# Kernel optimization log

Measured on AMD Instinct MI355X. Metric: run time of the kernel, lower is better.

The kernel has to match this reference:

```python
import jax, jax.numpy as jnp
import numpy as np

EPS = 1e-5  # torch LayerNorm default
H = 8       # heads_num


def _ln(t, g, b):
    m = jnp.mean(t, axis=-1, keepdims=True)
    v = jnp.var(t, axis=-1, keepdims=True)
    return (t - m) / jnp.sqrt(v + EPS) * g + b


def setup_inputs() -> dict:
    key = jax.random.key(0)
    ks = jax.random.split(key, 12)
    B, S, Dq, Dk, Dff = 4, 2048, 512, 768, 2048
    def w(k, shape, scale=0.02):
        return jax.random.normal(k, shape, jnp.float32) * scale
    return {
        "x": jax.random.normal(ks[0], (B, S, Dq), jnp.float32),
        "y": jax.random.normal(ks[1], (B, S, Dk), jnp.float32),
        # cross-attention projections (stored [in, out]; linear_q/k/v have no bias)
        "Wq": w(ks[2], (Dq, Dq)), "Wk": w(ks[3], (Dk, Dq)), "Wv": w(ks[4], (Dk, Dq)),
        "Wo": w(ks[5], (Dq, Dq)), "bo": jnp.zeros((Dq,), jnp.float32),
        # nn.MultiheadAttention packed in-projection and out-projection
        "mha_w_in": w(ks[6], (Dq, 3 * Dq)), "mha_b_in": jnp.zeros((3 * Dq,), jnp.float32),
        "mha_wo": w(ks[7], (Dq, Dq)), "mha_bo": jnp.zeros((Dq,), jnp.float32),
        # 4 LayerNorms
        "ln1_g": jnp.ones((Dq,), jnp.float32), "ln1_b": jnp.zeros((Dq,), jnp.float32),
        "ln2_g": jnp.ones((Dk,), jnp.float32), "ln2_b": jnp.zeros((Dk,), jnp.float32),
        "ln3_g": jnp.ones((Dq,), jnp.float32), "ln3_b": jnp.zeros((Dq,), jnp.float32),
        "ln4_g": jnp.ones((Dq,), jnp.float32), "ln4_b": jnp.zeros((Dq,), jnp.float32),
        # dense MLP (moe=False branch)
        "mlp_w1": w(ks[8], (Dq, Dff)), "mlp_b1": jnp.zeros((Dff,), jnp.float32),
        "mlp_w2": w(ks[9], (Dff, Dq)), "mlp_b2": jnp.zeros((Dq,), jnp.float32),
    }


def reference(x, y, Wq, Wk, Wv, Wo, bo, mha_w_in, mha_b_in, mha_wo, mha_bo,
              ln1_g, ln1_b, ln2_g, ln2_b, ln3_g, ln3_b, ln4_g, ln4_b,
              mlp_w1, mlp_b1, mlp_w2, mlp_b2):
    B, S, D = x.shape
    hd = D // H
    inv_sqrt_hd = 1.0 / np.sqrt(hd).astype(np.float32)

    xn = _ln(x, ln1_g, ln1_b)
    yn = _ln(y, ln2_g, ln2_b)

    # ---- Multi_CrossAttention: manual QK^T softmax V over true seq axis ----
    q = (xn @ Wq).reshape(B, S, H, hd)
    k = (yn @ Wk).reshape(B, -1, H, hd)
    v = (yn @ Wv).reshape(B, -1, H, hd)
    scores = jnp.einsum('bqhd,bkhd->bhqk', q, k) * inv_sqrt_hd  # [B,H,S,S] (512 MB)
    attn = jax.nn.softmax(scores, axis=-1)
    ctx = jnp.einsum('bhqk,bkhd->bqhd', attn, v).reshape(B, S, D)
    ca = ctx @ Wo + bo

    h = _ln(ca + xn, ln3_g, ln3_b)

    # ---- nn.MultiheadAttention (batch_first=False!): axis 0 is the sequence ----
    qkv = h @ mha_w_in + mha_b_in  # [L=B, N=S, 3D]
    q2, k2, v2 = jnp.split(qkv, 3, axis=-1)
    L, N = q2.shape[0], q2.shape[1]
    q2 = q2.reshape(L, N, H, hd)
    k2 = k2.reshape(L, N, H, hd)
    v2 = v2.reshape(L, N, H, hd)
    s2 = jnp.einsum('lnhd,mnhd->nhlm', q2, k2) * inv_sqrt_hd  # [N,H,L,L]
    a2 = jax.nn.softmax(s2, axis=-1)
    sa = jnp.einsum('nhlm,mnhd->lnhd', a2, v2).reshape(L, N, D) @ mha_wo + mha_bo

    h2 = _ln(sa + h, ln4_g, ln4_b)

    # ---- dense MLP (GELU exact, dropout=0) ----
    mlp = jax.nn.gelu(h2 @ mlp_w1 + mlp_b1, approximate=False) @ mlp_w2 + mlp_b2
    return mlp + h2
```

## Files before the change

### kernel.cpp

```cpp
#include <hip/hip_runtime.h>
#include <math.h>

typedef unsigned short u16;
typedef __attribute__((ext_vector_type(8))) short bf8;
typedef __attribute__((ext_vector_type(4))) float f4;
typedef __attribute__((ext_vector_type(16))) float f32x16;
typedef __attribute__((ext_vector_type(4))) unsigned int u32x4;
typedef __attribute__((ext_vector_type(2))) unsigned int u32x2;
typedef __attribute__((ext_vector_type(4))) unsigned short u16x4;
typedef __attribute__((ext_vector_type(8))) unsigned short u16x8;

__device__ __forceinline__ float bf2f(u16 a){
  unsigned u = ((unsigned)a) << 16;
  float f; __builtin_memcpy(&f, &u, 4);
  return f;
}
__device__ __forceinline__ u16 f2bf(float f){
  unsigned u; __builtin_memcpy(&u, &f, 4);
  u += 0x7fffu + ((u >> 16) & 1u);
  return (u16)(u >> 16);
}
__device__ __forceinline__ unsigned cvtpk(float a, float b){
  unsigned r;
  asm("v_cvt_pk_bf16_f32 %0, %1, %2" : "=v"(r) : "v"(a), "v"(b));
  return r;
}
__device__ __forceinline__ void plswap(unsigned &a, unsigned &b){
  asm("v_permlane32_swap_b32 %0, %1" : "+v"(a), "+v"(b));
}
__device__ __forceinline__ void gload16(const u16* g, u16* l){
  __builtin_amdgcn_global_load_lds((const __attribute__((address_space(1))) void*)g,
                                   (__attribute__((address_space(3))) void*)l, 16, 0, 0);
}
__device__ __forceinline__ int xcd_swizzle(int orig, int nwg){
  const int qq = nwg >> 3, rr = nwg & 7;
  const int xcd = orig & 7, loc = orig >> 3;
  return (xcd < rr ? xcd * (qq + 1) : rr * (qq + 1) + (xcd - rr) * qq) + loc;
}

__global__ void k_transpose_all(
    const float* __restrict__ Wq, const float* __restrict__ Wk,
    const float* __restrict__ Wv, const float* __restrict__ Wo,
    const float* __restrict__ Win, const float* __restrict__ Wmo,
    const float* __restrict__ W1, const float* __restrict__ W2,
    u16* __restrict__ WqT, u16* __restrict__ WkT, u16* __restrict__ WvT,
    u16* __restrict__ WoT, u16* __restrict__ WinT, u16* __restrict__ WmoT,
    u16* __restrict__ W1T, u16* __restrict__ W2T)
{
  __shared__ float tile[32][33];
  const int tid = blockIdx.x;
  const float* in; u16* out; int R, C, lo;
  if (tid < 1280){
    if (tid < 256)       { in = Wq;  out = WqT;  R = 512; C = 512;  lo = 0; }
    else if (tid < 640)  { in = Wk;  out = WkT;  R = 768; C = 512;  lo = 256; }
    else if (tid < 1024) { in = Wv;  out = WvT;  R = 768; C = 512;  lo = 640; }
    else                 { in = Wo;  out = WoT;  R = 512; C = 512;  lo = 1024; }
  } else {
    if (tid < 2048)      { in = Win; out = WinT; R = 512; C = 1536; lo = 1280; }
    else if (tid < 2304) { in = Wmo; out = WmoT; R = 512; C = 512;  lo = 2048; }
    else if (tid < 3328) { in = W1;  out = W1T;  R = 512; C = 2048; lo = 2304; }
    else                 { in = W2;  out = W2T;  R = 2048; C = 512; lo = 3328; }
  }
  const int local = tid - lo;
  const int tpx = C >> 5;
  const int bx = (local % tpx) * 32, by = (local / tpx) * 32;
  const int tx = threadIdx.x, ty = threadIdx.y;
#pragma unroll
  for (int i = 0; i < 4; i++)
    tile[ty + i*8][tx] = in[(size_t)(by + ty + i*8) * C + bx + tx];
  __syncthreads();
#pragma unroll
  for (int i = 0; i < 4; i++)
    out[(size_t)(bx + ty + i*8) * R + by + tx] = f2bf(tile[tx][ty + i*8]);
}

__device__ __forceinline__ void ln_row(
    const float* __restrict__ r, const float* __restrict__ gam,
    const float* __restrict__ bet, float* __restrict__ outf,
    u16* __restrict__ outb, int D, int t)
{
  const int nv = D >> 8;
  float v[3] = {0.f, 0.f, 0.f};
  float s = 0.f, s2 = 0.f;
#pragma unroll
  for (int i = 0; i < 3; i++){
    if (i < nv){ float xx = r[t + i*256]; v[i] = xx; s += xx; s2 += xx*xx; }
  }
#pragma unroll
  for (int m = 32; m; m >>= 1){ s += __shfl_xor(s, m); s2 += __shfl_xor(s2, m); }
  __shared__ float rs[4], rq[4];
  const int wave = t >> 6;
  if ((t & 63) == 0){ rs[wave] = s; rq[wave] = s2; }
  __syncthreads();
  s  = rs[0] + rs[1] + rs[2] + rs[3];
  s2 = rq[0] + rq[1] + rq[2] + rq[3];
  const float mean = s / (float)D;
  const float var  = s2 / (float)D - mean * mean;
  const float rstd = rsqrtf(var + 1e-5f);
#pragma unroll
  for (int i = 0; i < 3; i++){
    if (i < nv){
      const int c = t + i*256;
      float o = (v[i] - mean) * rstd * gam[c] + bet[c];
      if (outf) outf[c] = o;
      outb[c] = f2bf(o);
    }
  }
}

__global__ __launch_bounds__(256) void k_layernorm(
    const float* __restrict__ in, const float* __restrict__ gam,
    const float* __restrict__ bet, float* __restrict__ outf,
    u16* __restrict__ outb, int D)
{
  const int row = blockIdx.x;
  ln_row(in + (size_t)row * D, gam, bet,
         outf ? outf + (size_t)row * D : nullptr,
         outb + (size_t)row * D, D, threadIdx.x);
}

__global__ __launch_bounds__(256) void k_layernorm12(
    const float* __restrict__ x, const float* __restrict__ y,
    const float* __restrict__ g1, const float* __restrict__ b1,
    const float* __restrict__ g2, const float* __restrict__ b2,
    float* __restrict__ xnF, u16* __restrict__ xnB, u16* __restrict__ ynB)
{
  const int row = blockIdx.x;
  if (row < 8192){
    ln_row(x + (size_t)row * 512, g1, b1, xnF + (size_t)row * 512,
           xnB + (size_t)row * 512, 512, threadIdx.x);
  } else {
    const int r2 = row - 8192;
    ln_row(y + (size_t)r2 * 768, g2, b2, nullptr,
           ynB + (size_t)r2 * 768, 768, threadIdx.x);
  }
}

template<int TM, int TN, bool BIAS, bool RES, bool GELU_ACT, int OUTM, bool QSC = false>
__global__ __launch_bounds__(256, 4) void k_gemm(
    const u16* __restrict__ A, const u16* __restrict__ BT,
    const float* __restrict__ bias, const float* __restrict__ res,
    float* __restrict__ outf, u16* __restrict__ outb, u16* __restrict__ outb2,
    int M, int N, int K)
{
  constexpr int MF = TM / 32;
  constexpr int NF = TN / 32;
  constexpr int WM = TM / 2;
  constexpr int WN = TN / 2;
  __shared__ u16 Sb[(TM + TN) * 64];
  const int t = threadIdx.x;
  const int gx = gridDim.x;
  const int swz = xcd_swizzle(blockIdx.y * gx + blockIdx.x, gx * gridDim.y);
  const int m0 = (swz / gx) * TM, n0 = (swz % gx) * TN;
  const int wave = t >> 6, lane = t & 63;
  const int wm = wave >> 1, wn = wave & 1;
  const int l15 = lane & 15, lg = lane >> 4;
  const u16* Ag = A + (size_t)m0 * K;
  const u16* Bg = BT + (size_t)n0 * K;

  const int lrow = lane >> 3;
  const int csrc = (((lane & 7) ^ lrow) << 3);
  const u16* Agl = Ag + (size_t)lrow * K + csrc;
  const u16* Bgl = Bg + (size_t)lrow * K + csrc;

  f4 acc[MF][NF];
#pragma unroll
  for (int i = 0; i < MF; i++)
#pragma unroll
    for (int j = 0; j < NF; j++) acc[i][j] = (f4){0.f, 0.f, 0.f, 0.f};

  const int nK = K >> 6;
#pragma unroll
  for (int i = 0; i < TM/32; i++){
    const int rb = (i*4 + wave) * 8;
    gload16(Agl + (size_t)rb * K, &Sb[rb * 64]);
  }
#pragma unroll
  for (int i = 0; i < TN/32; i++){
    const int rb = (i*4 + wave) * 8;
    gload16(Bgl + (size_t)rb * K, &Sb[(TM + rb) * 64]);
  }
  asm volatile("s_waitcnt vmcnt(0)" ::: "memory");
  __syncthreads();

  for (int kt = 0;; kt++){
    const char* As = (const char*)&Sb[0];
    const char* Bs = (const char*)&Sb[TM * 64];
#pragma unroll
    for (int kc = 0; kc < 2; kc++){
      bf8 af[MF], bfr[NF];
      const int kb = kc*64 + lg*16;
#pragma unroll
      for (int mf = 0; mf < MF; mf++){
        const int row = wm*WM + mf*16 + l15;
        af[mf] = *(const bf8*)(As + row*128 + (kb ^ ((row & 7) << 4)));
      }
#pragma unroll
      for (int nf = 0; nf < NF; nf++){
        const int row = wn*WN + nf*16 + l15;
        bfr[nf] = *(const bf8*)(Bs + row*128 + (kb ^ ((row & 7) << 4)));
      }
#pragma unroll
      for (int mf = 0; mf < MF; mf++)
#pragma unroll
        for (int nf = 0; nf < NF; nf++)
          acc[mf][nf] = __builtin_amdgcn_mfma_f32_16x16x32_bf16(af[mf], bfr[nf], acc[mf][nf], 0, 0, 0);
    }
    if (kt + 1 == nK) break;
    __syncthreads();
    const int ko = (kt + 1) << 6;
#pragma unroll
    for (int i = 0; i < TM/32; i++){
      const int rb = (i*4 + wave) * 8;
      gload16(Agl + (size_t)rb * K + ko, &Sb[rb * 64]);
    }
#pragma unroll
    for (int i = 0; i < TN/32; i++){
      const int rb = (i*4 + wave) * 8;
      gload16(Bgl + (size_t)rb * K + ko, &Sb[(TM + rb) * 64]);
    }
    asm volatile("s_waitcnt vmcnt(0)" ::: "memory");
    __syncthreads();
  }
#pragma unroll
  for (int mf = 0; mf < MF; mf++){
#pragma unroll
    for (int nf = 0; nf < NF; nf++){
      const int colg = n0 + wn*WN + nf*16 + l15;
      const int rowg = m0 + wm*WM + mf*16 + lg*4;
      const float bv = BIAS ? bias[colg] : 0.f;
      float vv[4];
#pragma unroll
      for (int j = 0; j < 4; j++){
        float v = acc[mf][nf][j] + bv;
        if (RES) v += res[(size_t)(rowg + j) * N + colg];
        if (GELU_ACT) v = 0.5f * v * (1.f + erff(v * 0.7071067811865475f));
        if (QSC) v *= 0.1803368801f;
        vv[j] = v;
      }
      if (OUTM == 0){
#pragma unroll
        for (int j = 0; j < 4; j++) outf[(size_t)(rowg + j) * N + colg] = vv[j];
      } else if (OUTM == 1){
#pragma unroll
        for (int j = 0; j < 4; j++) outb[(size_t)(rowg + j) * N + colg] = f2bf(vv[j]);
      } else if (OUTM == 2){
        const int bb = rowg >> 11, ss = rowg & 2047;
        u16x4 pk;
#pragma unroll
        for (int j = 0; j < 4; j++) pk[j] = f2bf(vv[j]);
        *(u16x4*)(outb + ((size_t)(bb*512 + colg)) * 2048 + ss) = pk;
      } else {
        if (n0 < 512){
#pragma unroll
          for (int j = 0; j < 4; j++) outb[(size_t)(rowg + j) * 512 + colg] = f2bf(vv[j]);
        } else {
          const int bb = rowg >> 11, ss = rowg & 2047;
          u16x4 pk;
#pragma unroll
          for (int j = 0; j < 4; j++) pk[j] = f2bf(vv[j]);
          *(u16x4*)(outb2 + ((size_t)(bb*512 + (colg - 512))) * 2048 + ss) = pk;
        }
      }
    }
  }
}

__global__ __launch_bounds__(256, 2) void k_flash(
    const u16* __restrict__ q, const u16* __restrict__ k,
    const u16* __restrict__ vt, u16* __restrict__ ctx)
{
  __shared__ u16 Kb[2][64 * 64];
  __shared__ u16 Vb[2][64 * 64];
  const int t = threadIdx.x;
  const int wave = t >> 6, lane = t & 63;
  const int l31 = lane & 31, hi = lane >> 5;
  const int id = blockIdx.y * 16 + blockIdx.x;
  const int swz = xcd_swizzle(id, 512);
  const int qb = swz & 15, bh = swz >> 4;
  const int b = bh >> 3, h = bh & 7;
  const int qrow0 = qb*128 + wave*32;

  bf8 qf[4];
  {
    const u16* qp = q + ((size_t)(b*2048 + qrow0 + l31)) * 512 + h*64 + hi*8;
    qf[0] = *(const bf8*)qp;
    qf[1] = *(const bf8*)(qp + 16);
    qf[2] = *(const bf8*)(qp + 32);
    qf[3] = *(const bf8*)(qp + 48);
  }

  const int lrow = lane >> 3;
  const int csrc = (((lane & 7) ^ lrow) << 3);
  const u16* kgl = k  + ((size_t)(b*2048 + lrow)) * 512  + h*64 + csrc;
  const u16* vgl = vt + ((size_t)(b*512 + h*64 + lrow)) * 2048 + csrc;

#pragma unroll
  for (int i = 0; i < 2; i++){
    const int rb = (i*4 + wave) * 8;
    gload16(kgl + (size_t)rb * 512,  &Kb[0][rb * 64]);
    gload16(vgl + (size_t)rb * 2048, &Vb[0][rb * 64]);
  }

  f32x16 o0, o1;
#pragma unroll
  for (int r = 0; r < 16; r++){ o0[r] = 0.f; o1[r] = 0.f; }
  float rl = 0.f;

  int cur = 0;
  for (int it = 0; it < 32; it++){
    asm volatile("s_waitcnt vmcnt(0)" ::: "memory");
    __syncthreads();
    if (it + 1 < 32){
      const int kt = (it + 1) << 6;
#pragma unroll
      for (int i = 0; i < 2; i++){
        const int rb = (i*4 + wave) * 8;
        gload16(kgl + (size_t)(kt + rb) * 512,  &Kb[cur^1][rb * 64]);
        gload16(vgl + (size_t)rb * 2048 + kt,   &Vb[cur^1][rb * 64]);
      }
    }
    const char* kbuf = (const char*)Kb[cur];
    const char* vbuf = (const char*)Vb[cur];
    f32x16 s0, s1;
#pragma unroll
    for (int r = 0; r < 16; r++){ s0[r] = 0.f; s1[r] = 0.f; }
    __builtin_amdgcn_s_setprio(1);
#pragma unroll
    for (int ds = 0; ds < 4; ds++){
      const int off = ds*32 + hi*16;
      const int row0 = l31, row1 = 32 + l31;
      const bf8 kf0 = *(const bf8*)(kbuf + row0*128 + (off ^ ((row0 & 7) << 4)));
      const bf8 kf1 = *(const bf8*)(kbuf + row1*128 + (off ^ ((row1 & 7) << 4)));
      s0 = __builtin_amdgcn_mfma_f32_32x32x16_bf16(kf0, qf[ds], s0, 0, 0, 0);
      s1 = __builtin_amdgcn_mfma_f32_32x32x16_bf16(kf1, qf[ds], s1, 0, 0, 0);
    }
    __builtin_amdgcn_s_setprio(0);
    float p0[16], p1[16];
#pragma unroll
    for (int r = 0; r < 16; r++){
      p0[r] = __builtin_amdgcn_exp2f(s0[r]);
      p1[r] = __builtin_amdgcn_exp2f(s1[r]);
    }
    float sum = 0.f;
#pragma unroll
    for (int r = 0; r < 16; r++) sum += p0[r] + p1[r];
    sum += __shfl_xor(sum, 32);
    rl += sum;
    bf8 pa[2][2];
#pragma unroll
    for (int sub = 0; sub < 2; sub++){
      const float* pp = sub ? p1 : p0;
      unsigned w0 = cvtpk(pp[0],  pp[1]),  w1 = cvtpk(pp[2],  pp[3]);
      unsigned w2 = cvtpk(pp[4],  pp[5]),  w3 = cvtpk(pp[6],  pp[7]);
      unsigned w4 = cvtpk(pp[8],  pp[9]),  w5 = cvtpk(pp[10], pp[11]);
      unsigned w6 = cvtpk(pp[12], pp[13]), w7 = cvtpk(pp[14], pp[15]);
      plswap(w0, w2); plswap(w1, w3);
      plswap(w4, w6); plswap(w5, w7);
      u32x4 t0 = {w0, w1, w2, w3};
      u32x4 t1 = {w4, w5, w6, w7};
      __builtin_memcpy(&pa[sub][0], &t0, 16);
      __builtin_memcpy(&pa[sub][1], &t1, 16);
    }
    __builtin_amdgcn_s_setprio(1);
#pragma unroll
    for (int sub = 0; sub < 2; sub++)
#pragma unroll
      for (int kt2 = 0; kt2 < 2; kt2++){
        const int off = sub*64 + kt2*32 + hi*16;
        const int row0 = l31, row1 = 32 + l31;
        const bf8 vf0 = *(const bf8*)(vbuf + row0*128 + (off ^ ((row0 & 7) << 4)));
        const bf8 vf1 = *(const bf8*)(vbuf + row1*128 + (off ^ ((row1 & 7) << 4)));
        o0 = __builtin_amdgcn_mfma_f32_32x32x16_bf16(pa[sub][kt2], vf0, o0, 0, 0, 0);
        o1 = __builtin_amdgcn_mfma_f32_32x32x16_bf16(pa[sub][kt2], vf1, o1, 0, 0, 0);
      }
    __builtin_amdgcn_s_setprio(0);
    cur ^= 1;
  }
  const float linv = 1.f / rl;
#pragma unroll
  for (int r = 0; r < 16; r++){
    const int crow = (r & 3) + 8*(r >> 2) + 4*hi;
    const float iv = __shfl(linv, crow);
    u16* cp = ctx + ((size_t)(b*2048 + qrow0 + crow)) * 512 + h*64 + l31;
    cp[0]  = f2bf(o0[r] * iv);
    cp[32] = f2bf(o1[r] * iv);
  }
}

__global__ __launch_bounds__(256) void k_mha_small(const u16* __restrict__ qkv,
                                                   u16* __restrict__ outb)
{
  const int tid = blockIdx.x * 256 + threadIdx.x;
  const int n = tid & 2047;
  const int hl = tid >> 11;
  const int h = hl >> 2, l = hl & 3;
  const u16* qp = qkv + ((size_t)l * 2048 + n) * 1536 + h*64;
  float qv[64];
#pragma unroll
  for (int i = 0; i < 8; i++){
    const bf8 c = *(const bf8*)(qp + i*8);
#pragma unroll
    for (int j2 = 0; j2 < 8; j2++) qv[i*8 + j2] = bf2f((u16)c[j2]) * 0.125f;
  }
  float sc[4];
#pragma unroll
  for (int m = 0; m < 4; m++){
    const u16* kp = qkv + ((size_t)m * 2048 + n) * 1536 + 512 + h*64;
    float a = 0.f;
#pragma unroll
    for (int i = 0; i < 8; i++){
      const bf8 c = *(const bf8*)(kp + i*8);
#pragma unroll
      for (int j2 = 0; j2 < 8; j2++) a += qv[i*8 + j2] * bf2f((u16)c[j2]);
    }
    sc[m] = a;
  }
  const float mx = fmaxf(fmaxf(sc[0], sc[1]), fmaxf(sc[2], sc[3]));
  float p[4]; float sum = 0.f;
#pragma unroll
  for (int m = 0; m < 4; m++){ p[m] = __expf(sc[m] - mx); sum += p[m]; }
  const float inv = 1.f / sum;
  float ov[64];
#pragma unroll
  for (int i = 0; i < 64; i++) ov[i] = 0.f;
#pragma unroll
  for (int m = 0; m < 4; m++){
    const float pw = p[m] * inv;
    const u16* vp = qkv + ((size_t)m * 2048 + n) * 1536 + 1024 + h*64;
#pragma unroll
    for (int i = 0; i < 8; i++){
      const bf8 c = *(const bf8*)(vp + i*8);
#pragma unroll
      for (int j2 = 0; j2 < 8; j2++) ov[i*8 + j2] += pw * bf2f((u16)c[j2]);
    }
  }
  u16* op = outb + ((size_t)l * 2048 + n) * 512 + h*64;
#pragma unroll
  for (int i = 0; i < 8; i++){
    u16x8 pk;
#pragma unroll
    for (int j2 = 0; j2 < 8; j2++) pk[j2] = f2bf(ov[i*8 + j2]);
    *(u16x8*)(op + i*8) = pk;
  }
}

extern "C" void kernel_launch(void* const* d_in, const int* in_sizes, int n_in,
                              void* d_out, int out_size, void* d_ws, size_t ws_size,
                              hipStream_t stream)
{
  (void)in_sizes; (void)n_in; (void)out_size; (void)ws_size;
  const float* x    = (const float*)d_in[0];
  const float* y    = (const float*)d_in[1];
  const float* Wq   = (const float*)d_in[2];
  const float* Wk   = (const float*)d_in[3];
  const float* Wv   = (const float*)d_in[4];
  const float* Wo   = (const float*)d_in[5];
  const float* bo   = (const float*)d_in[6];
  const float* Win  = (const float*)d_in[7];
  const float* bin  = (const float*)d_in[8];
  const float* Wmo  = (const float*)d_in[9];
  const float* bmo  = (const float*)d_in[10];
  const float* ln1g = (const float*)d_in[11];
  const float* ln1b = (const float*)d_in[12];
  const float* ln2g = (const float*)d_in[13];
  const float* ln2b = (const float*)d_in[14];
  const float* ln3g = (const float*)d_in[15];
  const float* ln3b = (const float*)d_in[16];
  const float* ln4g = (const float*)d_in[17];
  const float* ln4b = (const float*)d_in[18];
  const float* W1   = (const float*)d_in[19];
  const float* b1   = (const float*)d_in[20];
  const float* W2   = (const float*)d_in[21];
  const float* b2   = (const float*)d_in[22];

  char* ws = (char*)d_ws;
  const size_t MB = 1024 * 1024;
  u16* WqT  = (u16*)ws;
  u16* WkT  = WqT  + 512 * 512;
  u16* WvT  = WkT  + 512 * 768;
  u16* WoT  = WvT  + 512 * 768;
  u16* WinT = WoT  + 512 * 512;
  u16* WmoT = WinT + 1536 * 512;
  u16* W1T  = WmoT + 512 * 512;
  u16* W2T  = W1T  + 2048 * 512;
  float* hF   = (float*)(ws + 9 * MB);
  float* xnF  = (float*)(ws + 25 * MB);
  float* carF = (float*)(ws + 41 * MB);
  u16* xnB  = (u16*)(ws + 57 * MB);
  u16* ynB  = (u16*)(ws + 65 * MB);
  u16* qB   = (u16*)(ws + 77 * MB);
  u16* kB   = (u16*)(ws + 85 * MB);
  u16* vtB  = (u16*)(ws + 93 * MB);
  u16* ctxB = (u16*)(ws + 101 * MB);
  float* sarF = xnF;
  float* h2F  = carF;
  u16* saB   = xnB;
  u16* hB    = ynB;
  u16* h2B   = qB;
  u16* qkvB  = kB;
  u16* t1B   = (u16*)hF;

  k_transpose_all<<<4352, dim3(32, 8), 0, stream>>>(
      Wq, Wk, Wv, Wo, Win, Wmo, W1, W2,
      WqT, WkT, WvT, WoT, WinT, WmoT, W1T, W2T);

  k_layernorm12<<<16384, 256, 0, stream>>>(x, y, ln1g, ln1b, ln2g, ln2b,
                                           xnF, xnB, ynB);

  k_gemm<64,128,false,false,false,1,true><<<dim3(4, 128), 256, 0, stream>>>(xnB, WqT, nullptr, nullptr, nullptr, qB, nullptr, 8192, 512, 512);
  k_gemm<64,128,false,false,false,3><<<dim3(8, 128), 256, 0, stream>>>(ynB, WkT, nullptr, nullptr, nullptr, kB, vtB,   8192, 1024, 768);

  k_flash<<<dim3(16, 32), 256, 0, stream>>>(qB, kB, vtB, ctxB);

  k_gemm<64,128,true,true,false,0><<<dim3(4, 128), 256, 0, stream>>>(ctxB, WoT, bo, xnF, carF, nullptr, nullptr, 8192, 512, 512);
  k_layernorm<<<8192, 256, 0, stream>>>(carF, ln3g, ln3b, hF, hB, 512);

  k_gemm<128,128,true,false,false,1><<<dim3(12, 64), 256, 0, stream>>>(hB, WinT, bin, nullptr, nullptr, qkvB, nullptr, 8192, 1536, 512);
  k_mha_small<<<256, 256, 0, stream>>>(qkvB, saB);
  k_gemm<64,128,true,true,false,0><<<dim3(4, 128), 256, 0, stream>>>(saB, WmoT, bmo, hF, sarF, nullptr, nullptr, 8192, 512, 512);
  k_layernorm<<<8192, 256, 0, stream>>>(sarF, ln4g, ln4b, h2F, h2B, 512);

  k_gemm<128,128,true,false,true,1><<<dim3(16, 64), 256, 0, stream>>>(h2B, W1T, b1, nullptr, nullptr, t1B, nullptr, 8192, 2048, 512);
  k_gemm<64,128,true,true,false,0><<<dim3(4, 128), 256, 0, stream>>>(t1B, W2T, b2, h2F, (float*)d_out, nullptr, nullptr, 8192, 512, 2048);
}
```

Before: 232.3 us.

## Triple-buffer GEMM shared-memory tiles and use 64x128 tiles for all GEMMs

```diff
diff --git a/kernel.cpp b/kernel.cpp
--- a/kernel.cpp
+++ b/kernel.cpp
@@ -137,7 +137,7 @@
 }
 
 template<int TM, int TN, bool BIAS, bool RES, bool GELU_ACT, int OUTM, bool QSC = false>
-__global__ __launch_bounds__(256, 4) void k_gemm(
+__global__ __launch_bounds__(256, 2) void k_gemm(
     const u16* __restrict__ A, const u16* __restrict__ BT,
     const float* __restrict__ bias, const float* __restrict__ res,
     float* __restrict__ outf, u16* __restrict__ outb, u16* __restrict__ outb2,
@@ -147,7 +147,8 @@
   constexpr int NF = TN / 32;
   constexpr int WM = TM / 2;
   constexpr int WN = TN / 2;
-  __shared__ u16 Sb[(TM + TN) * 64];
+  constexpr int BUFE = (TM + TN) * 64;
+  __shared__ u16 Sb[3 * BUFE];
   const int t = threadIdx.x;
   const int gx = gridDim.x;
   const int swz = xcd_swizzle(blockIdx.y * gx + blockIdx.x, gx * gridDim.y);
@@ -170,22 +171,36 @@
     for (int j = 0; j < NF; j++) acc[i][j] = (f4){0.f, 0.f, 0.f, 0.f};
 
   const int nK = K >> 6;
-#pragma unroll
-  for (int i = 0; i < TM/32; i++){
-    const int rb = (i*4 + wave) * 8;
-    gload16(Agl + (size_t)rb * K, &Sb[rb * 64]);
-  }
-#pragma unroll
-  for (int i = 0; i < TN/32; i++){
-    const int rb = (i*4 + wave) * 8;
-    gload16(Bgl + (size_t)rb * K, &Sb[(TM + rb) * 64]);
-  }
-  asm volatile("s_waitcnt vmcnt(0)" ::: "memory");
+
+  auto stage = [&](int kt, int bi){
+    u16* dst = &Sb[bi * BUFE];
+    const int ko = kt << 6;
+#pragma unroll
+    for (int i = 0; i < TM/32; i++){
+      const int rb = (i*4 + wave) * 8;
+      gload16(Agl + (size_t)rb * K + ko, dst + rb * 64);
+    }
+#pragma unroll
+    for (int i = 0; i < TN/32; i++){
+      const int rb = (i*4 + wave) * 8;
+      gload16(Bgl + (size_t)rb * K + ko, dst + (TM + rb) * 64);
+    }
+  };
+
+  stage(0, 0);
+  if (nK > 1){
+    stage(1, 1);
+    asm volatile("s_waitcnt vmcnt(6)" ::: "memory");
+  } else {
+    asm volatile("s_waitcnt vmcnt(0)" ::: "memory");
+  }
   __syncthreads();
 
+  int cb = 0, sbuf = 2;
   for (int kt = 0;; kt++){
-    const char* As = (const char*)&Sb[0];
-    const char* Bs = (const char*)&Sb[TM * 64];
+    if (kt + 2 < nK) stage(kt + 2, sbuf);
+    const char* As = (const char*)&Sb[cb * BUFE];
+    const char* Bs = (const char*)&Sb[cb * BUFE + TM * 64];
 #pragma unroll
     for (int kc = 0; kc < 2; kc++){
       bf8 af[MF], bfr[NF];
@@ -207,20 +222,11 @@
           acc[mf][nf] = __builtin_amdgcn_mfma_f32_16x16x32_bf16(af[mf], bfr[nf], acc[mf][nf], 0, 0, 0);
     }
     if (kt + 1 == nK) break;
+    if (kt + 2 < nK) asm volatile("s_waitcnt vmcnt(6)" ::: "memory");
+    else             asm volatile("s_waitcnt vmcnt(0)" ::: "memory");
     __syncthreads();
-    const int ko = (kt + 1) << 6;
-#pragma unroll
-    for (int i = 0; i < TM/32; i++){
-      const int rb = (i*4 + wave) * 8;
-      gload16(Agl + (size_t)rb * K + ko, &Sb[rb * 64]);
-    }
-#pragma unroll
-    for (int i = 0; i < TN/32; i++){
-      const int rb = (i*4 + wave) * 8;
-      gload16(Bgl + (size_t)rb * K + ko, &Sb[(TM + rb) * 64]);
-    }
-    asm volatile("s_waitcnt vmcnt(0)" ::: "memory");
-    __syncthreads();
+    cb   = (cb   == 2) ? 0 : cb + 1;
+    sbuf = (sbuf == 2) ? 0 : sbuf + 1;
   }
 #pragma unroll
   for (int mf = 0; mf < MF; mf++){
@@ -516,11 +522,11 @@
   k_gemm<64,128,true,true,false,0><<<dim3(4, 128), 256, 0, stream>>>(ctxB, WoT, bo, xnF, carF, nullptr, nullptr, 8192, 512, 512);
   k_layernorm<<<8192, 256, 0, stream>>>(carF, ln3g, ln3b, hF, hB, 512);
 
-  k_gemm<128,128,true,false,false,1><<<dim3(12, 64), 256, 0, stream>>>(hB, WinT, bin, nullptr, nullptr, qkvB, nullptr, 8192, 1536, 512);
+  k_gemm<64,128,true,false,false,1><<<dim3(12, 128), 256, 0, stream>>>(hB, WinT, bin, nullptr, nullptr, qkvB, nullptr, 8192, 1536, 512);
   k_mha_small<<<256, 256, 0, stream>>>(qkvB, saB);
   k_gemm<64,128,true,true,false,0><<<dim3(4, 128), 256, 0, stream>>>(saB, WmoT, bmo, hF, sarF, nullptr, nullptr, 8192, 512, 512);
   k_layernorm<<<8192, 256, 0, stream>>>(sarF, ln4g, ln4b, h2F, h2B, 512);
 
-  k_gemm<128,128,true,false,true,1><<<dim3(16, 64), 256, 0, stream>>>(h2B, W1T, b1, nullptr, nullptr, t1B, nullptr, 8192, 2048, 512);
+  k_gemm<64,128,true,false,true,1><<<dim3(16, 128), 256, 0, stream>>>(h2B, W1T, b1, nullptr, nullptr, t1B, nullptr, 8192, 2048, 512);
   k_gemm<64,128,true,true,false,0><<<dim3(4, 128), 256, 0, stream>>>(t1B, W2T, b2, h2F, (float*)d_out, nullptr, nullptr, 8192, 512, 2048);
 }
```

Result: slower. 241.7 us (+4.0%).

## Keep residual/LayerNorm intermediates in bf16 and use tanh-approx GELU

Applied to the files above, without the earlier changes.

```diff
diff --git a/kernel.cpp b/kernel.cpp
--- a/kernel.cpp
+++ b/kernel.cpp
@@ -36,6 +36,12 @@
   const int qq = nwg >> 3, rr = nwg & 7;
   const int xcd = orig & 7, loc = orig >> 3;
   return (xcd < rr ? xcd * (qq + 1) : rr * (qq + 1) + (xcd - rr) * qq) + loc;
+}
+__device__ __forceinline__ float gelu_f(float v){
+  const float vc = fminf(v, 10.f);
+  const float z  = vc * (1.f + 0.044715f * vc * vc);
+  const float e  = __builtin_amdgcn_exp2f(2.302208499f * z);
+  return v * e * __builtin_amdgcn_rcpf(e + 1.f);
 }
 
 __global__ void k_transpose_all(
@@ -74,10 +80,9 @@
     out[(size_t)(bx + ty + i*8) * R + by + tx] = f2bf(tile[tx][ty + i*8]);
 }
 
-__device__ __forceinline__ void ln_row(
+__device__ __forceinline__ void ln_row_f32(
     const float* __restrict__ r, const float* __restrict__ gam,
-    const float* __restrict__ bet, float* __restrict__ outf,
-    u16* __restrict__ outb, int D, int t)
+    const float* __restrict__ bet, u16* __restrict__ outb, int D, int t)
 {
   const int nv = D >> 8;
   float v[3] = {0.f, 0.f, 0.f};
@@ -101,45 +106,55 @@
   for (int i = 0; i < 3; i++){
     if (i < nv){
       const int c = t + i*256;
-      float o = (v[i] - mean) * rstd * gam[c] + bet[c];
-      if (outf) outf[c] = o;
-      outb[c] = f2bf(o);
-    }
-  }
-}
-
-__global__ __launch_bounds__(256) void k_layernorm(
-    const float* __restrict__ in, const float* __restrict__ gam,
-    const float* __restrict__ bet, float* __restrict__ outf,
-    u16* __restrict__ outb, int D)
-{
-  const int row = blockIdx.x;
-  ln_row(in + (size_t)row * D, gam, bet,
-         outf ? outf + (size_t)row * D : nullptr,
-         outb + (size_t)row * D, D, threadIdx.x);
+      outb[c] = f2bf((v[i] - mean) * rstd * gam[c] + bet[c]);
+    }
+  }
 }
 
 __global__ __launch_bounds__(256) void k_layernorm12(
     const float* __restrict__ x, const float* __restrict__ y,
     const float* __restrict__ g1, const float* __restrict__ b1,
     const float* __restrict__ g2, const float* __restrict__ b2,
-    float* __restrict__ xnF, u16* __restrict__ xnB, u16* __restrict__ ynB)
+    u16* __restrict__ xnB, u16* __restrict__ ynB)
 {
   const int row = blockIdx.x;
   if (row < 8192){
-    ln_row(x + (size_t)row * 512, g1, b1, xnF + (size_t)row * 512,
-           xnB + (size_t)row * 512, 512, threadIdx.x);
+    ln_row_f32(x + (size_t)row * 512, g1, b1, xnB + (size_t)row * 512, 512, threadIdx.x);
   } else {
     const int r2 = row - 8192;
-    ln_row(y + (size_t)r2 * 768, g2, b2, nullptr,
-           ynB + (size_t)r2 * 768, 768, threadIdx.x);
-  }
+    ln_row_f32(y + (size_t)r2 * 768, g2, b2, ynB + (size_t)r2 * 768, 768, threadIdx.x);
+  }
+}
+
+__global__ __launch_bounds__(256) void k_layernorm_b(
+    const u16* __restrict__ in, const float* __restrict__ gam,
+    const float* __restrict__ bet, u16* __restrict__ outb)
+{
+  const int row = blockIdx.x, t = threadIdx.x;
+  const u16* r = in + (size_t)row * 512;
+  const float v0 = bf2f(r[t]);
+  const float v1 = bf2f(r[t + 256]);
+  float s = v0 + v1, s2 = v0*v0 + v1*v1;
+#pragma unroll
+  for (int m = 32; m; m >>= 1){ s += __shfl_xor(s, m); s2 += __shfl_xor(s2, m); }
+  __shared__ float rs[4], rq[4];
+  const int wave = t >> 6;
+  if ((t & 63) == 0){ rs[wave] = s; rq[wave] = s2; }
+  __syncthreads();
+  s  = rs[0] + rs[1] + rs[2] + rs[3];
+  s2 = rq[0] + rq[1] + rq[2] + rq[3];
+  const float mean = s * (1.f / 512.f);
+  const float var  = s2 * (1.f / 512.f) - mean * mean;
+  const float rstd = rsqrtf(var + 1e-5f);
+  u16* o = outb + (size_t)row * 512;
+  o[t]       = f2bf((v0 - mean) * rstd * gam[t] + bet[t]);
+  o[t + 256] = f2bf((v1 - mean) * rstd * gam[t + 256] + bet[t + 256]);
 }
 
 template<int TM, int TN, bool BIAS, bool RES, bool GELU_ACT, int OUTM, bool QSC = false>
 __global__ __launch_bounds__(256, 4) void k_gemm(
     const u16* __restrict__ A, const u16* __restrict__ BT,
-    const float* __restrict__ bias, const float* __restrict__ res,
+    const float* __restrict__ bias, const u16* __restrict__ res,
     float* __restrict__ outf, u16* __restrict__ outb, u16* __restrict__ outb2,
     int M, int N, int K)
 {
@@ -233,8 +248,8 @@
 #pragma unroll
       for (int j = 0; j < 4; j++){
         float v = acc[mf][nf][j] + bv;
-        if (RES) v += res[(size_t)(rowg + j) * N + colg];
-        if (GELU_ACT) v = 0.5f * v * (1.f + erff(v * 0.7071067811865475f));
+        if (RES) v += bf2f(res[(size_t)(rowg + j) * N + colg]);
+        if (GELU_ACT) v = gelu_f(v);
         if (QSC) v *= 0.1803368801f;
         vv[j] = v;
       }
@@ -484,43 +499,39 @@
   u16* WmoT = WinT + 1536 * 512;
   u16* W1T  = WmoT + 512 * 512;
   u16* W2T  = W1T  + 2048 * 512;
-  float* hF   = (float*)(ws + 9 * MB);
-  float* xnF  = (float*)(ws + 25 * MB);
-  float* carF = (float*)(ws + 41 * MB);
-  u16* xnB  = (u16*)(ws + 57 * MB);
-  u16* ynB  = (u16*)(ws + 65 * MB);
-  u16* qB   = (u16*)(ws + 77 * MB);
-  u16* kB   = (u16*)(ws + 85 * MB);
-  u16* vtB  = (u16*)(ws + 93 * MB);
-  u16* ctxB = (u16*)(ws + 101 * MB);
-  float* sarF = xnF;
-  float* h2F  = carF;
-  u16* saB   = xnB;
-  u16* hB    = ynB;
-  u16* h2B   = qB;
-  u16* qkvB  = kB;
-  u16* t1B   = (u16*)hF;
+  u16* xnB  = (u16*)(ws +   9 * MB);
+  u16* ynB  = (u16*)(ws +  17 * MB);
+  u16* qB   = (u16*)(ws +  29 * MB);
+  u16* kB   = (u16*)(ws +  37 * MB);
+  u16* vtB  = (u16*)(ws +  45 * MB);
+  u16* ctxB = (u16*)(ws +  53 * MB);
+  u16* carB = (u16*)(ws +  61 * MB);
+  u16* hB   = (u16*)(ws +  69 * MB);
+  u16* qkvB = (u16*)(ws +  77 * MB);
+  u16* saB  = (u16*)(ws + 101 * MB);
+  u16* sarB = qB;
+  u16* h2B  = kB;
+  u16* t1B  = vtB;
 
   k_transpose_all<<<4352, dim3(32, 8), 0, stream>>>(
       Wq, Wk, Wv, Wo, Win, Wmo, W1, W2,
       WqT, WkT, WvT, WoT, WinT, WmoT, W1T, W2T);
 
-  k_layernorm12<<<16384, 256, 0, stream>>>(x, y, ln1g, ln1b, ln2g, ln2b,
-                                           xnF, xnB, ynB);
+  k_layernorm12<<<16384, 256, 0, stream>>>(x, y, ln1g, ln1b, ln2g, ln2b, xnB, ynB);
 
   k_gemm<64,128,false,false,false,1,true><<<dim3(4, 128), 256, 0, stream>>>(xnB, WqT, nullptr, nullptr, nullptr, qB, nullptr, 8192, 512, 512);
   k_gemm<64,128,false,false,false,3><<<dim3(8, 128), 256, 0, stream>>>(ynB, WkT, nullptr, nullptr, nullptr, kB, vtB,   8192, 1024, 768);
 
   k_flash<<<dim3(16, 32), 256, 0, stream>>>(qB, kB, vtB, ctxB);
 
-  k_gemm<64,128,true,true,false,0><<<dim3(4, 128), 256, 0, stream>>>(ctxB, WoT, bo, xnF, carF, nullptr, nullptr, 8192, 512, 512);
-  k_layernorm<<<8192, 256, 0, stream>>>(carF, ln3g, ln3b, hF, hB, 512);
+  k_gemm<64,128,true,true,false,1><<<dim3(4, 128), 256, 0, stream>>>(ctxB, WoT, bo, xnB, nullptr, carB, nullptr, 8192, 512, 512);
+  k_layernorm_b<<<8192, 256, 0, stream>>>(carB, ln3g, ln3b, hB);
 
   k_gemm<128,128,true,false,false,1><<<dim3(12, 64), 256, 0, stream>>>(hB, WinT, bin, nullptr, nullptr, qkvB, nullptr, 8192, 1536, 512);
   k_mha_small<<<256, 256, 0, stream>>>(qkvB, saB);
-  k_gemm<64,128,true,true,false,0><<<dim3(4, 128), 256, 0, stream>>>(saB, WmoT, bmo, hF, sarF, nullptr, nullptr, 8192, 512, 512);
-  k_layernorm<<<8192, 256, 0, stream>>>(sarF, ln4g, ln4b, h2F, h2B, 512);
+  k_gemm<64,128,true,true,false,1><<<dim3(4, 128), 256, 0, stream>>>(saB, WmoT, bmo, hB, nullptr, sarB, nullptr, 8192, 512, 512);
+  k_layernorm_b<<<8192, 256, 0, stream>>>(sarB, ln4g, ln4b, h2B);
 
   k_gemm<128,128,true,false,true,1><<<dim3(16, 64), 256, 0, stream>>>(h2B, W1T, b1, nullptr, nullptr, t1B, nullptr, 8192, 2048, 512);
-  k_gemm<64,128,true,true,false,0><<<dim3(4, 128), 256, 0, stream>>>(t1B, W2T, b2, h2F, (float*)d_out, nullptr, nullptr, 8192, 512, 2048);
-}
+  k_gemm<64,128,true,true,false,0><<<dim3(4, 128), 256, 0, stream>>>(t1B, W2T, b2, h2B, (float*)d_out, nullptr, nullptr, 8192, 512, 2048);
+}
```

After: 218.4 us. -6.0%, faster.
